# Kernel tuning notes

Measured on AMD Instinct MI355X. Metric: run time of the kernel, lower is better.

The kernel has to match this reference:

```python
import jax, jax.numpy as jnp
import numpy as np
from jax import lax

EPS = 1e-5

def _conv3x3(x, w):
    # x: [N,C,H,W], w: [O,I,3,3]
    return lax.conv_general_dilated(x, w, window_strides=(1, 1),
                                    padding=((1, 1), (1, 1)),
                                    dimension_numbers=('NCHW', 'OIHW', 'NCHW'))

def _bn(x, gamma, beta, mean, var):
    # inference-mode batchnorm, per-channel over dim 1
    scale = (gamma * lax.rsqrt(var + EPS))[None, :, None, None]
    shift = (beta - mean * gamma * lax.rsqrt(var + EPS))[None, :, None, None]
    return x * scale + shift

def setup_inputs() -> dict:
    key = jax.random.key(0)
    ks = jax.random.split(key, 11)
    N, C, H, W = 64, 128, 56, 56
    d = {}
    d['x'] = jax.random.normal(ks[0], (N, C, H, W), dtype=jnp.float32)
    d['w1'] = jax.random.normal(ks[1], (C, C, 3, 3), dtype=jnp.float32) * (1.0 / np.sqrt(9 * C))
    d['g1'] = jax.random.uniform(ks[2], (C,), dtype=jnp.float32, minval=0.5, maxval=1.5)
    d['b1'] = jax.random.normal(ks[3], (C,), dtype=jnp.float32) * 0.1
    d['m1'] = jax.random.normal(ks[4], (C,), dtype=jnp.float32) * 0.1
    d['v1'] = jax.random.uniform(ks[5], (C,), dtype=jnp.float32, minval=0.5, maxval=1.5)
    d['w2'] = jax.random.normal(ks[6], (C, C, 3, 3), dtype=jnp.float32) * (1.0 / np.sqrt(9 * C))
    d['g2'] = jax.random.uniform(ks[7], (C,), dtype=jnp.float32, minval=0.5, maxval=1.5)
    d['b2'] = jax.random.normal(ks[8], (C,), dtype=jnp.float32) * 0.1
    d['m2'] = jax.random.normal(ks[9], (C,), dtype=jnp.float32) * 0.1
    d['v2'] = jax.random.uniform(ks[10], (C,), dtype=jnp.float32, minval=0.5, maxval=1.5)
    return d

def reference(x, w1, g1, b1, m1, v1, w2, g2, b2, m2, v2):
    identity = x  # downsample is None (stride=1, inplanes==planes)
    out = _conv3x3(x, w1)
    out = jax.nn.relu(_bn(out, g1, b1, m1, v1))
    out = _conv3x3(out, w2)
    out = _bn(out, g2, b2, m2, v2)
    out = out + identity
    return jax.nn.relu(out)
```

## Files before the change

kernel.cpp:

```cpp
#include <hip/hip_runtime.h>
#include <hip/hip_bf16.h>

typedef __attribute__((ext_vector_type(8))) short short8;
typedef __attribute__((ext_vector_type(4))) float f32x4;

static constexpr int NN = 64;
static constexpr int C  = 128;
static constexpr int H  = 56;
static constexpr int W  = 56;
static constexpr int HP = 58;
static constexpr int ROWB = HP * 256;
static constexpr int XSLOT = 15360;

__device__ __forceinline__ void gload16(const void* g, void* l) {
    __builtin_amdgcn_global_load_lds(
        (const __attribute__((address_space(1))) unsigned int*)g,
        (__attribute__((address_space(3))) unsigned int*)l, 16, 0, 0);
}

__device__ __forceinline__ f32x4 mfma16(short8 a, short8 b, f32x4 c) {
    return __builtin_amdgcn_mfma_f32_16x16x32_bf16(a, b, c, 0, 0, 0);
}

__global__ __launch_bounds__(128)
void pack_weights(const float* __restrict__ w, const float* __restrict__ g,
                  const float* __restrict__ b, const float* __restrict__ m,
                  const float* __restrict__ v, __hip_bfloat16* __restrict__ Wp,
                  float* __restrict__ shift)
{
    int o = blockIdx.x;
    int c = threadIdx.x;
    float scale = g[o] * rsqrtf(v[o] + 1e-5f);
    if (c == 0) shift[o] = b[o] - m[o] * scale;
    const float* ws = w + ((size_t)o * C + c) * 9;
    int ks = c >> 5, lane = (o & 15) | (((c >> 3) & 3) << 4), jj = c & 7;
    int ob = o >> 4;
    #pragma unroll
    for (int tap = 0; tap < 9; ++tap) {
        size_t f = (size_t)(tap * 4 + ks) * 8 + ob;
        Wp[f * 512 + lane * 8 + jj] = __float2bfloat16(ws[tap] * scale);
    }
}

__global__ __launch_bounds__(256)
void transform_x(const float* __restrict__ x, __hip_bfloat16* __restrict__ Xp)
{
    __shared__ float t[C * 57];
    int bid = blockIdx.x;
    int n = bid / H, h = bid % H;
    int tid = threadIdx.x;

    #pragma unroll
    for (int i = 0; i < 7; ++i) {
        int idx4 = i * 256 + tid;
        int c  = idx4 / 14;
        int wq = (idx4 % 14) * 4;
        const float* p = x + ((size_t)(n * C + c)) * (H * W) + h * W + wq;
        float4 vv = *(const float4*)p;
        t[c * 57 + wq + 0] = vv.x;
        t[c * 57 + wq + 1] = vv.y;
        t[c * 57 + wq + 2] = vv.z;
        t[c * 57 + wq + 3] = vv.w;
    }
    __syncthreads();
    #pragma unroll
    for (int i = 0; i < 28; ++i) {
        int idx = i * 256 + tid;
        int c = idx & 127, w = idx >> 7;
        float vv = t[c * 57 + w];
        Xp[(((size_t)n * HP + (h + 1)) * HP + (w + 1)) * C + c] = __float2bfloat16(vv);
    }
}

__global__ __launch_bounds__(256)
void zero_halo(__hip_bfloat16* __restrict__ buf)
{
    int idx = blockIdx.x * 256 + threadIdx.x;
    int n = idx / (228 * 16);
    int rem = idx % (228 * 16);
    int p = rem >> 4, l = rem & 15;
    int y, xq;
    if (p < 58)       { y = 0;  xq = p; }
    else if (p < 116) { y = 57; xq = p - 58; }
    else { int q = p - 116; y = 1 + (q >> 1); xq = (q & 1) * 57; }
    short8* dst = (short8*)(buf + (((size_t)n * HP + y) * HP + xq) * C + l * 8);
    *dst = short8{0,0,0,0,0,0,0,0};
}

template<int WHICH>
__global__ __launch_bounds__(512, 2)
void conv3x3_kernel(const __hip_bfloat16* __restrict__ Xp,
                    const __hip_bfloat16* __restrict__ Wp,
                    const float* __restrict__ shift,
                    const float* __restrict__ ident,
                    void* __restrict__ outp)
{
    __shared__ char s_x[3 * XSLOT + 2048];
    __shared__ char s_w[3][8192];

    const int tid  = threadIdx.x;
    const int wave = tid >> 6;
    const int lane = tid & 63;
    const int lr   = lane & 15;
    const int lg   = lane >> 4;
    const int wm   = wave >> 2;
    const int mh   = (wave >> 1) & 1;
    const int oh   = wave & 1;

    const int bid0 = blockIdx.x;
    const int bid  = (bid0 & 7) * 224 + (bid0 >> 3);
    const int n = bid / 28, h0 = (bid % 28) * 2;

    const char* xbase = (const char*)Xp + ((size_t)n * HP + h0) * ROWB;
    const char* wbase = (const char*)Wp;

    #pragma unroll
    for (int i = 0; i < 6; ++i) {
        int u = wave + i * 8;
        if (u < 45) {
            int q = u / 15, blk = u % 15;
            int d = blk * 1024 + lane * 16;
            int s = d ^ (((d >> 8) & 15) << 4);
            gload16(xbase + (size_t)q * ROWB + s, s_x + q * XSLOT + d);
        }
    }
    gload16(wbase + tid * 16, s_w[0] + tid * 16);
    gload16(wbase + 8192 + tid * 16, s_w[1] + tid * 16);

    f32x4 acc[2][4];
    #pragma unroll
    for (int i = 0; i < 2; ++i)
        #pragma unroll
        for (int j = 0; j < 4; ++j)
            acc[i][j] = f32x4{0.f, 0.f, 0.f, 0.f};

    __syncthreads();

    #pragma unroll
    for (int s = 0; s < 36; ++s) {
        if (s < 34)
            gload16(wbase + (size_t)(s + 2) * 8192 + tid * 16,
                    s_w[(s + 2) % 3] + tid * 16);
        if (s == 12) {
            #pragma unroll
            for (int i = 0; i < 2; ++i) {
                int u = wave + i * 8;
                if (u < 15) {
                    int d = u * 1024 + lane * 16;
                    int sw = d ^ (((d >> 8) & 15) << 4);
                    gload16(xbase + (size_t)3 * ROWB + sw, s_x + d);
                }
            }
        }
        const int tap = s >> 2, ks = s & 3;
        const int kh = tap / 3, kw = tap % 3;
        const int sbase = ((kh + wm) % 3) * XSLOT;
        const int cb = ks * 64 + lg * 16;
        const char* wcur = s_w[s % 3];

        short8 wb[4];
        #pragma unroll
        for (int of = 0; of < 4; ++of)
            wb[of] = *(const short8*)(wcur + (oh * 4 + of) * 1024 + lane * 16);
        short8 xa[2];
        #pragma unroll
        for (int mf = 0; mf < 2; ++mf) {
            int row = mh * 32 + mf * 16 + lr + kw;
            int off = (row * 256 + cb) ^ ((row & 15) << 4);
            xa[mf] = *(const short8*)(s_x + sbase + off);
        }
        __builtin_amdgcn_s_setprio(1);
        #pragma unroll
        for (int mf = 0; mf < 2; ++mf)
            #pragma unroll
            for (int of = 0; of < 4; ++of) {
                if (WHICH == 0)
                    acc[mf][of] = mfma16(xa[mf], wb[of], acc[mf][of]);
                else
                    acc[mf][of] = mfma16(wb[of], xa[mf], acc[mf][of]);
            }
        __builtin_amdgcn_s_setprio(0);

        if (s < 35) {
            __builtin_amdgcn_sched_barrier(0);
            if (s == 34)
                asm volatile("s_waitcnt vmcnt(0)" ::: "memory");
            else
                asm volatile("s_waitcnt vmcnt(1)" ::: "memory");
            __builtin_amdgcn_s_barrier();
            __builtin_amdgcn_sched_barrier(0);
        }
    }

    if (WHICH == 0) {
        __hip_bfloat16* o1 = (__hip_bfloat16*)outp;
        size_t rowb = ((size_t)n * HP + (h0 + wm + 1)) * HP;
        #pragma unroll
        for (int of = 0; of < 4; ++of) {
            int o = oh * 64 + of * 16 + lr;
            float sh = shift[o];
            #pragma unroll
            for (int mf = 0; mf < 2; ++mf) {
                #pragma unroll
                for (int r = 0; r < 4; ++r) {
                    int m = mh * 32 + mf * 16 + lg * 4 + r;
                    if (m < W) {
                        float f = acc[mf][of][r] + sh;
                        f = f > 0.f ? f : 0.f;
                        o1[(rowb + m + 1) * C + o] = __float2bfloat16(f);
                    }
                }
            }
        }
    } else {
        float* o2 = (float*)outp;
        int h = h0 + wm;
        #pragma unroll
        for (int mf = 0; mf < 2; ++mf) {
            int m = mh * 32 + mf * 16 + lr;
            if (m < W) {
                #pragma unroll
                for (int of = 0; of < 4; ++of) {
                    int ob = oh * 64 + of * 16 + lg * 4;
                    f32x4 sh = *(const f32x4*)(shift + ob);
                    #pragma unroll
                    for (int r = 0; r < 4; ++r) {
                        int o = ob + r;
                        size_t idx = ((size_t)(n * C + o) * H + h) * W + m;
                        float f = acc[mf][of][r] + sh[r] + ident[idx];
                        o2[idx] = f > 0.f ? f : 0.f;
                    }
                }
            }
        }
    }
}

extern "C" void kernel_launch(void* const* d_in, const int* in_sizes, int n_in,
                              void* d_out, int out_size, void* d_ws, size_t ws_size,
                              hipStream_t stream)
{
    const float* x  = (const float*)d_in[0];
    const float* w1 = (const float*)d_in[1];
    const float* g1 = (const float*)d_in[2];
    const float* b1 = (const float*)d_in[3];
    const float* m1 = (const float*)d_in[4];
    const float* v1 = (const float*)d_in[5];
    const float* w2 = (const float*)d_in[6];
    const float* g2 = (const float*)d_in[7];
    const float* b2 = (const float*)d_in[8];
    const float* m2 = (const float*)d_in[9];
    const float* v2 = (const float*)d_in[10];
    float* out = (float*)d_out;

    char* ws = (char*)d_ws;
    const size_t PADBUF = (size_t)NN * HP * HP * C * 2;
    const size_t WBUF   = (size_t)288 * 1024;
    size_t oX  = 0;
    size_t oY  = oX + PADBUF + 32768;
    size_t oW1 = oY + PADBUF + 32768;
    size_t oW2 = oW1 + WBUF;
    size_t oS1 = oW2 + WBUF;
    size_t oS2 = oS1 + 512;

    __hip_bfloat16* Xp  = (__hip_bfloat16*)(ws + oX);
    __hip_bfloat16* Y1  = (__hip_bfloat16*)(ws + oY);
    __hip_bfloat16* W1p = (__hip_bfloat16*)(ws + oW1);
    __hip_bfloat16* W2p = (__hip_bfloat16*)(ws + oW2);
    float* s1 = (float*)(ws + oS1);
    float* s2 = (float*)(ws + oS2);

    zero_halo<<<912, 256, 0, stream>>>(Xp);
    zero_halo<<<912, 256, 0, stream>>>(Y1);

    pack_weights<<<128, 128, 0, stream>>>(w1, g1, b1, m1, v1, W1p, s1);
    pack_weights<<<128, 128, 0, stream>>>(w2, g2, b2, m2, v2, W2p, s2);
    transform_x<<<NN * H, 256, 0, stream>>>(x, Xp);

    conv3x3_kernel<0><<<NN * 28, 512, 0, stream>>>(Xp, W1p, s1, nullptr, (void*)Y1);
    conv3x3_kernel<1><<<NN * 28, 512, 0, stream>>>(Y1, W2p, s2, x, (void*)out);
}
```

Measured before the change: 238.3 us.

## Store activations as per-row channel-block planes and read conv inputs straight from global

The padded activation buffers move from NHWC to per-row planes split into four 32-channel blocks, so each lane's MFMA fragment is a contiguous 16-byte load. The conv kernel no longer stages input rows in LDS; it loads fragments directly from global memory each k-step and keeps LDS only for the weight triple buffer. This removes the LDS staging traffic and swizzle, and lowers LDS use. In exchange every fragment is a global or cache load on the critical path, and the vmcnt waits now also count these loads, which changes how the weight prefetch is synchronised.

```diff
diff --git a/kernel.cpp b/kernel.cpp
--- a/kernel.cpp
+++ b/kernel.cpp
@@ -9,8 +9,9 @@
 static constexpr int H  = 56;
 static constexpr int W  = 56;
 static constexpr int HP = 58;
-static constexpr int ROWB = HP * 256;
-static constexpr int XSLOT = 15360;
+static constexpr int PLB  = 58 * 64;
+static constexpr int ROWB2 = 4 * PLB;
+static constexpr int NB   = 58 * ROWB2;
 
 __device__ __forceinline__ void gload16(const void* g, void* l) {
     __builtin_amdgcn_global_load_lds(
@@ -43,7 +44,7 @@
 }
 
 __global__ __launch_bounds__(256)
-void transform_x(const float* __restrict__ x, __hip_bfloat16* __restrict__ Xp)
+void transform_x(const float* __restrict__ x, char* __restrict__ Xp)
 {
     __shared__ float t[C * 57];
     int bid = blockIdx.x;
@@ -63,39 +64,50 @@
         t[c * 57 + wq + 3] = vv.w;
     }
     __syncthreads();
+    char* rowb = Xp + (size_t)n * NB + (size_t)(h + 1) * ROWB2;
     #pragma unroll
     for (int i = 0; i < 28; ++i) {
         int idx = i * 256 + tid;
         int c = idx & 127, w = idx >> 7;
         float vv = t[c * 57 + w];
-        Xp[(((size_t)n * HP + (h + 1)) * HP + (w + 1)) * C + c] = __float2bfloat16(vv);
+        int ks = c >> 5, cc = c & 31;
+        *(__hip_bfloat16*)(rowb + ks * PLB + (w + 1) * 64 + cc * 2) =
+            __float2bfloat16(vv);
     }
 }
 
 __global__ __launch_bounds__(256)
-void zero_halo(__hip_bfloat16* __restrict__ buf)
+void zero_halo(char* __restrict__ buf)
 {
     int idx = blockIdx.x * 256 + threadIdx.x;
-    int n = idx / (228 * 16);
-    int rem = idx % (228 * 16);
-    int p = rem >> 4, l = rem & 15;
-    int y, xq;
-    if (p < 58)       { y = 0;  xq = p; }
-    else if (p < 116) { y = 57; xq = p - 58; }
-    else { int q = p - 116; y = 1 + (q >> 1); xq = (q & 1) * 57; }
-    short8* dst = (short8*)(buf + (((size_t)n * HP + y) * HP + xq) * C + l * 8);
-    *dst = short8{0,0,0,0,0,0,0,0};
+    int n = idx / 3648, u = idx % 3648;
+    int y, ks, x, q;
+    if (u < 1856) {
+        y = (u < 928) ? 0 : 57;
+        int up = u % 928;
+        ks = up / 232;
+        int u2 = up % 232;
+        x = u2 >> 2; q = u2 & 3;
+    } else {
+        int v = u - 1856;
+        y = 1 + v / 32;
+        int vp = v % 32;
+        ks = vp >> 3;
+        int v2 = vp & 7;
+        x = (v2 >> 2) * 57; q = v2 & 3;
+    }
+    char* dst = buf + (size_t)n * NB + (size_t)y * ROWB2 + ks * PLB + x * 64 + q * 16;
+    *(short8*)dst = short8{0,0,0,0,0,0,0,0};
 }
 
 template<int WHICH>
 __global__ __launch_bounds__(512, 2)
-void conv3x3_kernel(const __hip_bfloat16* __restrict__ Xp,
+void conv3x3_kernel(const char* __restrict__ Xp,
                     const __hip_bfloat16* __restrict__ Wp,
                     const float* __restrict__ shift,
                     const float* __restrict__ ident,
                     void* __restrict__ outp)
 {
-    __shared__ char s_x[3 * XSLOT + 2048];
     __shared__ char s_w[3][8192];
 
     const int tid  = threadIdx.x;
@@ -111,19 +123,10 @@
     const int bid  = (bid0 & 7) * 224 + (bid0 >> 3);
     const int n = bid / 28, h0 = (bid % 28) * 2;
 
-    const char* xbase = (const char*)Xp + ((size_t)n * HP + h0) * ROWB;
+    const char* xn = Xp + (size_t)n * NB + (size_t)(h0 + wm) * ROWB2
+                   + (mh * 32 + lr) * 64 + lg * 16;
     const char* wbase = (const char*)Wp;
 
-    #pragma unroll
-    for (int i = 0; i < 6; ++i) {
-        int u = wave + i * 8;
-        if (u < 45) {
-            int q = u / 15, blk = u % 15;
-            int d = blk * 1024 + lane * 16;
-            int s = d ^ (((d >> 8) & 15) << 4);
-            gload16(xbase + (size_t)q * ROWB + s, s_x + q * XSLOT + d);
-        }
-    }
     gload16(wbase + tid * 16, s_w[0] + tid * 16);
     gload16(wbase + 8192 + tid * 16, s_w[1] + tid * 16);
 
@@ -134,41 +137,30 @@
         for (int j = 0; j < 4; ++j)
             acc[i][j] = f32x4{0.f, 0.f, 0.f, 0.f};
 
-    __syncthreads();
+    asm volatile("s_waitcnt vmcnt(1)" ::: "memory");
+    __builtin_amdgcn_s_barrier();
 
     #pragma unroll
     for (int s = 0; s < 36; ++s) {
+        const int tap = s >> 2, ks = s & 3;
+        const int kh = tap / 3, kw = tap % 3;
+
+        short8 xa[2];
+        #pragma unroll
+        for (int mf = 0; mf < 2; ++mf)
+            xa[mf] = *(const short8*)(xn + kh * ROWB2 + ks * PLB
+                                      + (mf * 16 + kw) * 64);
         if (s < 34)
             gload16(wbase + (size_t)(s + 2) * 8192 + tid * 16,
                     s_w[(s + 2) % 3] + tid * 16);
-        if (s == 12) {
-            #pragma unroll
-            for (int i = 0; i < 2; ++i) {
-                int u = wave + i * 8;
-                if (u < 15) {
-                    int d = u * 1024 + lane * 16;
-                    int sw = d ^ (((d >> 8) & 15) << 4);
-                    gload16(xbase + (size_t)3 * ROWB + sw, s_x + d);
-                }
-            }
-        }
-        const int tap = s >> 2, ks = s & 3;
-        const int kh = tap / 3, kw = tap % 3;
-        const int sbase = ((kh + wm) % 3) * XSLOT;
-        const int cb = ks * 64 + lg * 16;
+        __builtin_amdgcn_sched_barrier(0);
+
         const char* wcur = s_w[s % 3];
-
         short8 wb[4];
         #pragma unroll
         for (int of = 0; of < 4; ++of)
             wb[of] = *(const short8*)(wcur + (oh * 4 + of) * 1024 + lane * 16);
-        short8 xa[2];
-        #pragma unroll
-        for (int mf = 0; mf < 2; ++mf) {
-            int row = mh * 32 + mf * 16 + lr + kw;
-            int off = (row * 256 + cb) ^ ((row & 15) << 4);
-            xa[mf] = *(const short8*)(s_x + sbase + off);
-        }
+
         __builtin_amdgcn_s_setprio(1);
         #pragma unroll
         for (int mf = 0; mf < 2; ++mf)
@@ -183,22 +175,18 @@
 
         if (s < 35) {
             __builtin_amdgcn_sched_barrier(0);
-            if (s == 34)
-                asm volatile("s_waitcnt vmcnt(0)" ::: "memory");
-            else
-                asm volatile("s_waitcnt vmcnt(1)" ::: "memory");
             __builtin_amdgcn_s_barrier();
             __builtin_amdgcn_sched_barrier(0);
         }
     }
 
     if (WHICH == 0) {
-        __hip_bfloat16* o1 = (__hip_bfloat16*)outp;
-        size_t rowb = ((size_t)n * HP + (h0 + wm + 1)) * HP;
+        char* ybase = (char*)outp + (size_t)n * NB + (size_t)(h0 + wm + 1) * ROWB2;
         #pragma unroll
         for (int of = 0; of < 4; ++of) {
             int o = oh * 64 + of * 16 + lr;
             float sh = shift[o];
+            char* pl = ybase + (oh * 2 + (of >> 1)) * PLB + ((of & 1) * 16 + lr) * 2;
             #pragma unroll
             for (int mf = 0; mf < 2; ++mf) {
                 #pragma unroll
@@ -207,7 +195,7 @@
                     if (m < W) {
                         float f = acc[mf][of][r] + sh;
                         f = f > 0.f ? f : 0.f;
-                        o1[(rowb + m + 1) * C + o] = __float2bfloat16(f);
+                        *(__hip_bfloat16*)(pl + (m + 1) * 64) = __float2bfloat16(f);
                     }
                 }
             }
@@ -254,7 +242,7 @@
     float* out = (float*)d_out;
 
     char* ws = (char*)d_ws;
-    const size_t PADBUF = (size_t)NN * HP * HP * C * 2;
+    const size_t PADBUF = (size_t)NN * NB;
     const size_t WBUF   = (size_t)288 * 1024;
     size_t oX  = 0;
     size_t oY  = oX + PADBUF + 32768;
@@ -263,8 +251,8 @@
     size_t oS1 = oW2 + WBUF;
     size_t oS2 = oS1 + 512;
 
-    __hip_bfloat16* Xp  = (__hip_bfloat16*)(ws + oX);
-    __hip_bfloat16* Y1  = (__hip_bfloat16*)(ws + oY);
+    char* Xp  = ws + oX;
+    char* Y1  = ws + oY;
     __hip_bfloat16* W1p = (__hip_bfloat16*)(ws + oW1);
     __hip_bfloat16* W2p = (__hip_bfloat16*)(ws + oW2);
     float* s1 = (float*)(ws + oS1);
```

Measured after the change: 278.7 us. 16.9% more time.
